# Performance work log

Measured on AMD Instinct MI355X. Metric: run time of the kernel, lower is better.

The kernel has to match this reference:

```python
import jax, jax.numpy as jnp
from jax import lax
import numpy as np

B, L1, L2 = 64, 1024, 1024


def setup_inputs() -> dict:
    key = jax.random.key(0)
    ks = jax.random.split(key, 6)
    s1 = 1.0 / np.sqrt(L1)
    s2 = 1.0 / np.sqrt(L2)
    return {
        "a": jax.random.normal(ks[0], (B, L1), dtype=jnp.float32),
        "b": jax.random.normal(ks[1], (B, L2), dtype=jnp.float32),
        # nn.Linear(L1, L1) and nn.Linear(L2, L2) params (PyTorch default uniform init range)
        "W1": jax.random.uniform(ks[2], (L1, L1), jnp.float32, -s1, s1),
        "b1": jax.random.uniform(ks[3], (L1,), jnp.float32, -s1, s1),
        "W2": jax.random.uniform(ks[4], (L2, L2), jnp.float32, -s2, s2),
        "b2": jax.random.uniform(ks[5], (L2,), jnp.float32, -s2, s2),
    }


def _dtw_cost(cost):
    """DTW accumulated-cost DP for one [N, M] pairwise-cost matrix.

    R[i,j] = cost[i,j] + min(R[i-1,j-1], R[i-1,j], R[i,j-1]).
    The within-row dependency x[j] = c[j] + min(m[j], x[j-1]) is a min-plus
    prefix: x[j] = S[j] + cummin(m - S_{j-1}) with S = cumsum(c), which lets
    each row be computed in parallel (wavefront-equivalent vectorization).
    Returns the scalar DTW distance R[N-1, M-1].
    """
    dt = cost.dtype
    row0 = jnp.cumsum(cost[0])  # R[0, :]

    def step(prev_row, c_row):
        # m[j] = min(R[i-1, j], R[i-1, j-1]);  j=0 has no (i-1, j-1) neighbor
        shifted = jnp.concatenate([jnp.full((1,), jnp.inf, dt), prev_row[:-1]])
        m = jnp.minimum(prev_row, shifted)
        S = jnp.cumsum(c_row)
        S_prev = jnp.concatenate([jnp.zeros((1,), dt), S[:-1]])
        row = S + lax.associative_scan(jnp.minimum, m - S_prev)
        return row, None

    last_row, _ = lax.scan(step, row0, cost[1:])
    return last_row[-1]


def reference(a, b, W1, b1, W2, b2):
    # seq1 / seq2 linear projections over the time axis
    a_p = a @ W1.T + b1  # [B, L1]
    b_p = b @ W2.T + b2  # [B, L2]
    # squared-euclidean pairwise cost (scipy.sqeuclidean on scalar elements)
    cost = (a_p[:, :, None] - b_p[:, None, :]) ** 2  # [B, L1, L2]
    return jax.vmap(_dtw_cost)(cost)  # [B] DTW distances
```

## Files before the change

### kernel.cpp

```cpp
#include <hip/hip_runtime.h>
#include <math.h>


#define L 1024
#define BATCH 64

__global__ __launch_bounds__(256) void proj_kernel(
    const float* __restrict__ a, const float* __restrict__ b,
    const float* __restrict__ W1, const float* __restrict__ b1,
    const float* __restrict__ W2, const float* __restrict__ b2,
    float* __restrict__ ap, float* __restrict__ bp, int KC) {
  int part = blockIdx.x >> 7;
  int sub = blockIdx.x & 127;
  const float* X;
  const float* W;
  const float* bias;
  float* out;
  int i0;
  if (sub < 64) {
    X = a; W = W1; bias = b1; out = ap + part * BATCH * L; i0 = sub * 16;
  } else {
    X = b; W = W2; bias = b2; out = bp + part * BATCH * L; i0 = (sub - 64) * 16;
  }

  __shared__ float a_s[64][36];
  __shared__ float w_s[16][36];

  int tid = threadIdx.x;
  int lane_b = tid & 63;
  int iq = tid >> 6;

  float acc[4] = {0.f, 0.f, 0.f, 0.f};

  int kbeg = part * KC;
  int kend = kbeg + KC;
  for (int k0 = kbeg; k0 < kend; k0 += 32) {
    {
      int row = tid >> 2;
      int kl = (tid & 3) * 8;
      const float4* src = reinterpret_cast<const float4*>(&X[row * L + k0 + kl]);
      float4 v0 = src[0];
      float4 v1 = src[1];
      *reinterpret_cast<float4*>(&a_s[row][kl]) = v0;
      *reinterpret_cast<float4*>(&a_s[row][kl + 4]) = v1;
    }
    {
      int row = tid >> 4;
      int kl = (tid & 15) * 2;
      float2 v = *reinterpret_cast<const float2*>(&W[(i0 + row) * L + k0 + kl]);
      w_s[row][kl] = v.x;
      w_s[row][kl + 1] = v.y;
    }
    __syncthreads();
    #pragma unroll
    for (int kl = 0; kl < 32; kl += 4) {
      float4 av = *reinterpret_cast<const float4*>(&a_s[lane_b][kl]);
      #pragma unroll
      for (int m = 0; m < 4; ++m) {
        float4 wv = *reinterpret_cast<const float4*>(&w_s[iq * 4 + m][kl]);
        acc[m] += av.x * wv.x + av.y * wv.y + av.z * wv.z + av.w * wv.w;
      }
    }
    __syncthreads();
  }

  #pragma unroll
  for (int m = 0; m < 4; ++m) {
    int i = i0 + iq * 4 + m;
    float bv = (part == 0) ? bias[i] : 0.f;
    out[lane_b * L + i] = acc[m] + bv;
  }
}


#define NW 4
#define CPL 4
#define KBAR 32
#define OFF 95
#define DMAX (OFF * (NW - 1) + 63)
#define NG 43
#define NSTEPS (NG * KBAR)
#define APPAD (DMAX + NSTEPS + 64)

__device__ __forceinline__ float dpp_shr1_z(float v) {
  int r = __builtin_amdgcn_update_dpp(0, __float_as_int(v), 0x138, 0xf, 0xf,
                                      true);
  return __int_as_float(r);
}

__device__ __forceinline__ float dpp_shl1_z(float v) {
  int r = __builtin_amdgcn_update_dpp(0, __float_as_int(v), 0x130, 0xf, 0xf,
                                      true);
  return __int_as_float(r);
}

__device__ __forceinline__ float min3f(float x, float y, float z) {
  float r;
  asm("v_min3_f32 %0, %1, %2, %3" : "=v"(r) : "v"(x), "v"(y), "v"(z));
  return r;
}

__global__ __launch_bounds__(256, 1) void dtw_kernel(
    const float* __restrict__ app, const float* __restrict__ bpp,
    float* __restrict__ out, int parts) {
  const int b = blockIdx.x;
  const int tid = threadIdx.x;
  const int w = tid >> 6;
  const int t = tid & 63;
  const int woff = w * OFF;
  const int D = woff + t;
  const float INF = INFINITY;

  __shared__ float ap_pad[APPAD];
  __shared__ float ring[NW - 1][64];

  for (int idx = tid; idx < APPAD; idx += 256) {
    int src = idx - DMAX;
    float v = 0.f;
    if ((unsigned)src < (unsigned)L) {
      v = app[b * L + src];
      for (int p = 1; p < parts; ++p) v += app[p * BATCH * L + b * L + src];
    }
    ap_pad[idx] = v;
  }

  float4 bv = *reinterpret_cast<const float4*>(&bpp[b * L + tid * CPL]);
  for (int p = 1; p < parts; ++p) {
    float4 u = *reinterpret_cast<const float4*>(
        &bpp[p * BATCH * L + b * L + tid * CPL]);
    bv.x += u.x; bv.y += u.y; bv.z += u.z; bv.w += u.w;
  }
  const float bpv0 = bv.x, bpv1 = bv.y, bpv2 = bv.z, bpv3 = bv.w;

  float p0 = INF, p1 = INF, p2 = INF, p3 = INF;
  float right = INF, prev_left = INF;
  float vprod = INF;
  float ringchunk = INF;
  float apv = 0.f;
  float apchunk = 0.f;
  const bool lane0 = (t == 0);
  const bool lane63 = (t == 63);
  const int ap_base = DMAX - woff + t;

  __syncthreads();

#define DTW_GROUP(s0v, PRED, FIRSTG)                                         \
  {                                                                          \
    const int s0 = (s0v);                                                    \
    apchunk = ap_pad[ap_base + s0];                                          \
    if (w == 0)                                                              \
      ringchunk = ((FIRSTG) && lane0) ? 0.f : INF;                           \
    else if (t < KBAR)                                                       \
      ringchunk = ring[w - 1][(s0 - woff + t) & 63];                         \
    _Pragma("unroll")                                                        \
    for (int k = 0; k < KBAR; ++k) {                                         \
      float shifted = dpp_shr1_z(right);                                     \
      float left = lane0 ? ringchunk : shifted;                              \
      ringchunk = dpp_shl1_z(ringchunk);                                     \
      float apsh = dpp_shr1_z(apv);                                          \
      apv = lane0 ? apchunk : apsh;                                          \
      apchunk = dpp_shl1_z(apchunk);                                         \
      int ii = s0 + k - D;                                                   \
      if (!(PRED) || ((unsigned)ii < (unsigned)L)) {                         \
        float dprev = prev_left;                                             \
        if ((FIRSTG) && k == 1 && w == 0 && t == 0) dprev = INF;             \
        prev_left = left;                                                    \
        float d0 = apv - bpv0, d1 = apv - bpv1;                              \
        float d2 = apv - bpv2, d3 = apv - bpv3;                              \
        float x = left, bb;                                                  \
        bb = min3f(p0, dprev, x); x = __builtin_fmaf(d0, d0, bb);            \
        dprev = p0; p0 = x;                                                  \
        bb = min3f(p1, dprev, x); x = __builtin_fmaf(d1, d1, bb);            \
        dprev = p1; p1 = x;                                                  \
        bb = min3f(p2, dprev, x); x = __builtin_fmaf(d2, d2, bb);            \
        dprev = p2; p2 = x;                                                  \
        bb = min3f(p3, dprev, x); x = __builtin_fmaf(d3, d3, bb);            \
        p3 = x;                                                              \
        right = x;                                                           \
      }                                                                      \
      vprod = dpp_shl1_z(vprod);                                             \
      vprod = lane63 ? right : vprod;                                        \
    }                                                                        \
    if (w < NW - 1 && t >= 64 - KBAR)                                        \
      ring[w][(s0 + t - woff - (63 + KBAR)) & 63] = vprod;                   \
    __syncthreads();                                                         \
  }

  for (int g = 0; g < 11; ++g) DTW_GROUP(g * KBAR, true, g == 0);
  for (int g = 11; g < 32; ++g) DTW_GROUP(g * KBAR, false, false);
  for (int g = 32; g < NG; ++g) DTW_GROUP(g * KBAR, true, false);
#undef DTW_GROUP

  if (tid == NW * 64 - 1) out[b] = right;
}

extern "C" void kernel_launch(void* const* d_in, const int* in_sizes, int n_in,
                              void* d_out, int out_size, void* d_ws, size_t ws_size,
                              hipStream_t stream) {
  const float* a  = (const float*)d_in[0];
  const float* b  = (const float*)d_in[1];
  const float* W1 = (const float*)d_in[2];
  const float* b1 = (const float*)d_in[3];
  const float* W2 = (const float*)d_in[4];
  const float* b2 = (const float*)d_in[5];
  float* out = (float*)d_out;

  size_t per_part = (size_t)2 * BATCH * L * sizeof(float);
  int parts = 1;
  if (ws_size >= 4 * per_part) parts = 4;
  else if (ws_size >= 2 * per_part) parts = 2;

  float* ap = (float*)d_ws;
  float* bp = ap + (size_t)parts * BATCH * L;

  proj_kernel<<<128 * parts, 256, 0, stream>>>(a, b, W1, b1, W2, b2,
                                               ap, bp, L / parts);
  dtw_kernel<<<BATCH, 256, 0, stream>>>(ap, bp, out, parts);
}
```

Before: 101.3 us.

## Use min-plus prefix form for per-lane DTW cells and preload ap values

Rewrites the four-cell serial min3+fma chain per lane as a min-plus prefix computation, cumsum of costs plus a cummin of shifted minima. This shortens the dependency chain through the incoming left value so only the last min+add depends on the neighbour lane. It also drops the per-step DPP shifting of the a-projection value and instead loads all KBAR values for a group from shared memory into registers up front. The cost is more instructions per step, more register pressure, and slightly different float rounding because the subtract-then-add reassociation is not exact.

```diff
diff --git a/kernel.cpp b/kernel.cpp
--- a/kernel.cpp
+++ b/kernel.cpp
@@ -94,12 +94,6 @@
   return __int_as_float(r);
 }
 
-__device__ __forceinline__ float min3f(float x, float y, float z) {
-  float r;
-  asm("v_min3_f32 %0, %1, %2, %3" : "=v"(r) : "v"(x), "v"(y), "v"(z));
-  return r;
-}
-
 __global__ __launch_bounds__(256, 1) void dtw_kernel(
     const float* __restrict__ app, const float* __restrict__ bpp,
     float* __restrict__ out, int parts) {
@@ -136,18 +130,18 @@
   float right = INF, prev_left = INF;
   float vprod = INF;
   float ringchunk = INF;
-  float apv = 0.f;
-  float apchunk = 0.f;
   const bool lane0 = (t == 0);
   const bool lane63 = (t == 63);
-  const int ap_base = DMAX - woff + t;
+  const float* apl = &ap_pad[DMAX - D];
 
   __syncthreads();
 
 #define DTW_GROUP(s0v, PRED, FIRSTG)                                         \
   {                                                                          \
     const int s0 = (s0v);                                                    \
-    apchunk = ap_pad[ap_base + s0];                                          \
+    float apf[KBAR];                                                         \
+    _Pragma("unroll")                                                        \
+    for (int k = 0; k < KBAR; ++k) apf[k] = apl[s0 + k];                     \
     if (w == 0)                                                              \
       ringchunk = ((FIRSTG) && lane0) ? 0.f : INF;                           \
     else if (t < KBAR)                                                       \
@@ -157,26 +151,31 @@
       float shifted = dpp_shr1_z(right);                                     \
       float left = lane0 ? ringchunk : shifted;                              \
       ringchunk = dpp_shl1_z(ringchunk);                                     \
-      float apsh = dpp_shr1_z(apv);                                          \
-      apv = lane0 ? apchunk : apsh;                                          \
-      apchunk = dpp_shl1_z(apchunk);                                         \
       int ii = s0 + k - D;                                                   \
       if (!(PRED) || ((unsigned)ii < (unsigned)L)) {                         \
         float dprev = prev_left;                                             \
         if ((FIRSTG) && k == 1 && w == 0 && t == 0) dprev = INF;             \
         prev_left = left;                                                    \
+        float apv = apf[k];                                                  \
         float d0 = apv - bpv0, d1 = apv - bpv1;                              \
         float d2 = apv - bpv2, d3 = apv - bpv3;                              \
-        float x = left, bb;                                                  \
-        bb = min3f(p0, dprev, x); x = __builtin_fmaf(d0, d0, bb);            \
-        dprev = p0; p0 = x;                                                  \
-        bb = min3f(p1, dprev, x); x = __builtin_fmaf(d1, d1, bb);            \
-        dprev = p1; p1 = x;                                                  \
-        bb = min3f(p2, dprev, x); x = __builtin_fmaf(d2, d2, bb);            \
-        dprev = p2; p2 = x;                                                  \
-        bb = min3f(p3, dprev, x); x = __builtin_fmaf(d3, d3, bb);            \
-        p3 = x;                                                              \
-        right = x;                                                           \
+        float c0 = d0 * d0, c1 = d1 * d1, c2 = d2 * d2, c3 = d3 * d3;        \
+        float S0 = c0, S1 = S0 + c1, S2 = S1 + c2, S3 = S2 + c3;             \
+        float m0 = fminf(p0, dprev);                                         \
+        float m1 = fminf(p1, p0);                                            \
+        float m2 = fminf(p2, p1);                                            \
+        float m3 = fminf(p3, p2);                                            \
+        float z0 = m0;                                                       \
+        float z1 = m1 - S0, z2 = m2 - S1, z3 = m3 - S2;                      \
+        float u01 = fminf(z0, z1);                                           \
+        float v23 = fminf(z2, z3);                                           \
+        float cm2 = fminf(u01, z2);                                          \
+        float cm3 = fminf(u01, v23);                                         \
+        p0 = S0 + fminf(z0, left);                                           \
+        p1 = S1 + fminf(u01, left);                                          \
+        p2 = S2 + fminf(cm2, left);                                          \
+        p3 = S3 + fminf(cm3, left);                                          \
+        right = p3;                                                          \
       }                                                                      \
       vprod = dpp_shl1_z(vprod);                                             \
       vprod = lane63 ? right : vprod;                                        \
```

Result: slower. 131.2 us (+29.5%).

## Interleave two batch DTW problems per block and load ap from LDS directly

Applied to the files above, without the earlier changes.

Each DTW block now processes two batch elements at once, interleaving their independent dependency chains so the latency of each serial min3/fma chain can be overlapped by the other. The per-step DPP shift of the a-projection value is replaced by per-lane LDS reads of a 32-entry chunk into registers. The change halves the grid to 32 blocks and roughly doubles register and LDS use per block, so GPU occupancy drops further.

```diff
diff --git a/kernel.cpp b/kernel.cpp
--- a/kernel.cpp
+++ b/kernel.cpp
@@ -103,7 +103,8 @@
 __global__ __launch_bounds__(256, 1) void dtw_kernel(
     const float* __restrict__ app, const float* __restrict__ bpp,
     float* __restrict__ out, int parts) {
-  const int b = blockIdx.x;
+  const int bA = blockIdx.x * 2;
+  const int bB = bA + 1;
   const int tid = threadIdx.x;
   const int w = tid >> 6;
   const int t = tid & 63;
@@ -111,78 +112,114 @@
   const int D = woff + t;
   const float INF = INFINITY;
 
-  __shared__ float ap_pad[APPAD];
-  __shared__ float ring[NW - 1][64];
+  __shared__ float ap_pad[2][APPAD];
+  __shared__ float ring[2][NW - 1][64];
 
   for (int idx = tid; idx < APPAD; idx += 256) {
     int src = idx - DMAX;
-    float v = 0.f;
+    float vA = 0.f, vB = 0.f;
     if ((unsigned)src < (unsigned)L) {
-      v = app[b * L + src];
-      for (int p = 1; p < parts; ++p) v += app[p * BATCH * L + b * L + src];
-    }
-    ap_pad[idx] = v;
-  }
-
-  float4 bv = *reinterpret_cast<const float4*>(&bpp[b * L + tid * CPL]);
+      vA = app[bA * L + src];
+      vB = app[bB * L + src];
+      for (int p = 1; p < parts; ++p) {
+        vA += app[p * BATCH * L + bA * L + src];
+        vB += app[p * BATCH * L + bB * L + src];
+      }
+    }
+    ap_pad[0][idx] = vA;
+    ap_pad[1][idx] = vB;
+  }
+
+  float4 bvA = *reinterpret_cast<const float4*>(&bpp[bA * L + tid * CPL]);
+  float4 bvB = *reinterpret_cast<const float4*>(&bpp[bB * L + tid * CPL]);
   for (int p = 1; p < parts; ++p) {
-    float4 u = *reinterpret_cast<const float4*>(
-        &bpp[p * BATCH * L + b * L + tid * CPL]);
-    bv.x += u.x; bv.y += u.y; bv.z += u.z; bv.w += u.w;
-  }
-  const float bpv0 = bv.x, bpv1 = bv.y, bpv2 = bv.z, bpv3 = bv.w;
-
-  float p0 = INF, p1 = INF, p2 = INF, p3 = INF;
-  float right = INF, prev_left = INF;
-  float vprod = INF;
-  float ringchunk = INF;
-  float apv = 0.f;
-  float apchunk = 0.f;
+    float4 uA = *reinterpret_cast<const float4*>(
+        &bpp[p * BATCH * L + bA * L + tid * CPL]);
+    float4 uB = *reinterpret_cast<const float4*>(
+        &bpp[p * BATCH * L + bB * L + tid * CPL]);
+    bvA.x += uA.x; bvA.y += uA.y; bvA.z += uA.z; bvA.w += uA.w;
+    bvB.x += uB.x; bvB.y += uB.y; bvB.z += uB.z; bvB.w += uB.w;
+  }
+  const float bpv0A = bvA.x, bpv1A = bvA.y, bpv2A = bvA.z, bpv3A = bvA.w;
+  const float bpv0B = bvB.x, bpv1B = bvB.y, bpv2B = bvB.z, bpv3B = bvB.w;
+
+  float p0A = INF, p1A = INF, p2A = INF, p3A = INF;
+  float p0B = INF, p1B = INF, p2B = INF, p3B = INF;
+  float rightA = INF, prev_leftA = INF, vprodA = INF, ringchunkA = INF;
+  float rightB = INF, prev_leftB = INF, vprodB = INF, ringchunkB = INF;
   const bool lane0 = (t == 0);
   const bool lane63 = (t == 63);
-  const int ap_base = DMAX - woff + t;
+  const float* aplA = &ap_pad[0][DMAX - D];
+  const float* aplB = &ap_pad[1][DMAX - D];
 
   __syncthreads();
 
 #define DTW_GROUP(s0v, PRED, FIRSTG)                                         \
   {                                                                          \
     const int s0 = (s0v);                                                    \
-    apchunk = ap_pad[ap_base + s0];                                          \
-    if (w == 0)                                                              \
-      ringchunk = ((FIRSTG) && lane0) ? 0.f : INF;                           \
-    else if (t < KBAR)                                                       \
-      ringchunk = ring[w - 1][(s0 - woff + t) & 63];                         \
+    float apfA[KBAR], apfB[KBAR];                                            \
     _Pragma("unroll")                                                        \
     for (int k = 0; k < KBAR; ++k) {                                         \
-      float shifted = dpp_shr1_z(right);                                     \
-      float left = lane0 ? ringchunk : shifted;                              \
-      ringchunk = dpp_shl1_z(ringchunk);                                     \
-      float apsh = dpp_shr1_z(apv);                                          \
-      apv = lane0 ? apchunk : apsh;                                          \
-      apchunk = dpp_shl1_z(apchunk);                                         \
+      apfA[k] = aplA[s0 + k];                                                \
+      apfB[k] = aplB[s0 + k];                                                \
+    }                                                                        \
+    if (w == 0) {                                                            \
+      ringchunkA = ((FIRSTG) && lane0) ? 0.f : INF;                          \
+      ringchunkB = ((FIRSTG) && lane0) ? 0.f : INF;                          \
+    } else if (t < KBAR) {                                                   \
+      ringchunkA = ring[0][w - 1][(s0 - woff + t) & 63];                     \
+      ringchunkB = ring[1][w - 1][(s0 - woff + t) & 63];                     \
+    }                                                                        \
+    _Pragma("unroll")                                                        \
+    for (int k = 0; k < KBAR; ++k) {                                         \
+      float shiftedA = dpp_shr1_z(rightA);                                   \
+      float shiftedB = dpp_shr1_z(rightB);                                   \
+      float leftA = lane0 ? ringchunkA : shiftedA;                           \
+      float leftB = lane0 ? ringchunkB : shiftedB;                           \
+      ringchunkA = dpp_shl1_z(ringchunkA);                                   \
+      ringchunkB = dpp_shl1_z(ringchunkB);                                   \
       int ii = s0 + k - D;                                                   \
       if (!(PRED) || ((unsigned)ii < (unsigned)L)) {                         \
-        float dprev = prev_left;                                             \
-        if ((FIRSTG) && k == 1 && w == 0 && t == 0) dprev = INF;             \
-        prev_left = left;                                                    \
-        float d0 = apv - bpv0, d1 = apv - bpv1;                              \
-        float d2 = apv - bpv2, d3 = apv - bpv3;                              \
-        float x = left, bb;                                                  \
-        bb = min3f(p0, dprev, x); x = __builtin_fmaf(d0, d0, bb);            \
-        dprev = p0; p0 = x;                                                  \
-        bb = min3f(p1, dprev, x); x = __builtin_fmaf(d1, d1, bb);            \
-        dprev = p1; p1 = x;                                                  \
-        bb = min3f(p2, dprev, x); x = __builtin_fmaf(d2, d2, bb);            \
-        dprev = p2; p2 = x;                                                  \
-        bb = min3f(p3, dprev, x); x = __builtin_fmaf(d3, d3, bb);            \
-        p3 = x;                                                              \
-        right = x;                                                           \
+        float dprevA = prev_leftA;                                           \
+        float dprevB = prev_leftB;                                           \
+        if ((FIRSTG) && k == 1 && w == 0 && t == 0) {                        \
+          dprevA = INF;                                                      \
+          dprevB = INF;                                                      \
+        }                                                                    \
+        prev_leftA = leftA;                                                  \
+        prev_leftB = leftB;                                                  \
+        float apvA = apfA[k], apvB = apfB[k];                                \
+        float d0A = apvA - bpv0A, d1A = apvA - bpv1A;                        \
+        float d2A = apvA - bpv2A, d3A = apvA - bpv3A;                        \
+        float d0B = apvB - bpv0B, d1B = apvB - bpv1B;                        \
+        float d2B = apvB - bpv2B, d3B = apvB - bpv3B;                        \
+        float xA = leftA, xB = leftB, bbA, bbB;                              \
+        bbA = min3f(p0A, dprevA, xA); xA = __builtin_fmaf(d0A, d0A, bbA);    \
+        bbB = min3f(p0B, dprevB, xB); xB = __builtin_fmaf(d0B, d0B, bbB);    \
+        dprevA = p0A; p0A = xA;                                              \
+        dprevB = p0B; p0B = xB;                                              \
+        bbA = min3f(p1A, dprevA, xA); xA = __builtin_fmaf(d1A, d1A, bbA);    \
+        bbB = min3f(p1B, dprevB, xB); xB = __builtin_fmaf(d1B, d1B, bbB);    \
+        dprevA = p1A; p1A = xA;                                              \
+        dprevB = p1B; p1B = xB;                                              \
+        bbA = min3f(p2A, dprevA, xA); xA = __builtin_fmaf(d2A, d2A, bbA);    \
+        bbB = min3f(p2B, dprevB, xB); xB = __builtin_fmaf(d2B, d2B, bbB);    \
+        dprevA = p2A; p2A = xA;                                              \
+        dprevB = p2B; p2B = xB;                                              \
+        bbA = min3f(p3A, dprevA, xA); xA = __builtin_fmaf(d3A, d3A, bbA);    \
+        bbB = min3f(p3B, dprevB, xB); xB = __builtin_fmaf(d3B, d3B, bbB);    \
+        p3A = xA; rightA = xA;                                               \
+        p3B = xB; rightB = xB;                                               \
       }                                                                      \
-      vprod = dpp_shl1_z(vprod);                                             \
-      vprod = lane63 ? right : vprod;                                        \
-    }                                                                        \
-    if (w < NW - 1 && t >= 64 - KBAR)                                        \
-      ring[w][(s0 + t - woff - (63 + KBAR)) & 63] = vprod;                   \
+      vprodA = dpp_shl1_z(vprodA);                                           \
+      vprodB = dpp_shl1_z(vprodB);                                           \
+      vprodA = lane63 ? rightA : vprodA;                                     \
+      vprodB = lane63 ? rightB : vprodB;                                     \
+    }                                                                        \
+    if (w < NW - 1 && t >= 64 - KBAR) {                                      \
+      ring[0][w][(s0 + t - woff - (63 + KBAR)) & 63] = vprodA;               \
+      ring[1][w][(s0 + t - woff - (63 + KBAR)) & 63] = vprodB;               \
+    }                                                                        \
     __syncthreads();                                                         \
   }
 
@@ -191,7 +228,10 @@
   for (int g = 32; g < NG; ++g) DTW_GROUP(g * KBAR, true, false);
 #undef DTW_GROUP
 
-  if (tid == NW * 64 - 1) out[b] = right;
+  if (tid == NW * 64 - 1) {
+    out[bA] = rightA;
+    out[bB] = rightB;
+  }
 }
 
 extern "C" void kernel_launch(void* const* d_in, const int* in_sizes, int n_in,
@@ -215,5 +255,5 @@
 
   proj_kernel<<<128 * parts, 256, 0, stream>>>(a, b, W1, b1, W2, b2,
                                                ap, bp, L / parts);
-  dtw_kernel<<<BATCH, 256, 0, stream>>>(ap, bp, out, parts);
-}
+  dtw_kernel<<<BATCH / 2, 256, 0, stream>>>(ap, bp, out, parts);
+}
```

Result: slower. 148.4 us (+46.4%).

## Pack two DTW batches per block and load ap values directly from LDS

Applied to the files above, without the earlier changes.

The DTW kernel now runs two batch elements per 512-thread block (32 blocks instead of 64), each half using its own LDS ap buffer and ring. The per-step DPP shifting of ap values is replaced by loading 32 ap values per group straight from shared memory into registers. This trims the DPP and select work in the serial inner loop, but the block-wide barriers now couple two independent problems. It also halves the number of CUs in use and raises register pressure from the 32-element array.

```diff
diff --git a/kernel.cpp b/kernel.cpp
--- a/kernel.cpp
+++ b/kernel.cpp
@@ -100,34 +100,44 @@
   return r;
 }
 
-__global__ __launch_bounds__(256, 1) void dtw_kernel(
+__global__ __launch_bounds__(512, 1) void dtw_kernel(
     const float* __restrict__ app, const float* __restrict__ bpp,
     float* __restrict__ out, int parts) {
-  const int b = blockIdx.x;
   const int tid = threadIdx.x;
-  const int w = tid >> 6;
+  const int q = tid >> 8;
+  const int wl = (tid >> 6) & 3;
   const int t = tid & 63;
-  const int woff = w * OFF;
+  const int bq = blockIdx.x * 2 + q;
+  const int woff = wl * OFF;
   const int D = woff + t;
   const float INF = INFINITY;
 
-  __shared__ float ap_pad[APPAD];
-  __shared__ float ring[NW - 1][64];
-
-  for (int idx = tid; idx < APPAD; idx += 256) {
-    int src = idx - DMAX;
-    float v = 0.f;
-    if ((unsigned)src < (unsigned)L) {
-      v = app[b * L + src];
-      for (int p = 1; p < parts; ++p) v += app[p * BATCH * L + b * L + src];
-    }
-    ap_pad[idx] = v;
-  }
-
-  float4 bv = *reinterpret_cast<const float4*>(&bpp[b * L + tid * CPL]);
+  __shared__ float ap_pad[2][APPAD];
+  __shared__ float ring[2][NW - 1][64];
+
+  {
+    const int bA = blockIdx.x * 2;
+    for (int idx = tid; idx < APPAD; idx += 512) {
+      int src = idx - DMAX;
+      float vA = 0.f, vB = 0.f;
+      if ((unsigned)src < (unsigned)L) {
+        vA = app[bA * L + src];
+        vB = app[(bA + 1) * L + src];
+        for (int p = 1; p < parts; ++p) {
+          vA += app[p * BATCH * L + bA * L + src];
+          vB += app[p * BATCH * L + (bA + 1) * L + src];
+        }
+      }
+      ap_pad[0][idx] = vA;
+      ap_pad[1][idx] = vB;
+    }
+  }
+
+  const int colb = (tid & 255) * CPL;
+  float4 bv = *reinterpret_cast<const float4*>(&bpp[bq * L + colb]);
   for (int p = 1; p < parts; ++p) {
     float4 u = *reinterpret_cast<const float4*>(
-        &bpp[p * BATCH * L + b * L + tid * CPL]);
+        &bpp[p * BATCH * L + bq * L + colb]);
     bv.x += u.x; bv.y += u.y; bv.z += u.z; bv.w += u.w;
   }
   const float bpv0 = bv.x, bpv1 = bv.y, bpv2 = bv.z, bpv3 = bv.w;
@@ -136,35 +146,33 @@
   float right = INF, prev_left = INF;
   float vprod = INF;
   float ringchunk = INF;
-  float apv = 0.f;
-  float apchunk = 0.f;
   const bool lane0 = (t == 0);
   const bool lane63 = (t == 63);
-  const int ap_base = DMAX - woff + t;
+  const float* apl = &ap_pad[q][DMAX - D];
 
   __syncthreads();
 
 #define DTW_GROUP(s0v, PRED, FIRSTG)                                         \
   {                                                                          \
     const int s0 = (s0v);                                                    \
-    apchunk = ap_pad[ap_base + s0];                                          \
-    if (w == 0)                                                              \
+    float apf[KBAR];                                                         \
+    _Pragma("unroll")                                                        \
+    for (int k = 0; k < KBAR; ++k) apf[k] = apl[s0 + k];                     \
+    if (wl == 0)                                                             \
       ringchunk = ((FIRSTG) && lane0) ? 0.f : INF;                           \
     else if (t < KBAR)                                                       \
-      ringchunk = ring[w - 1][(s0 - woff + t) & 63];                         \
+      ringchunk = ring[q][wl - 1][(s0 - woff + t) & 63];                     \
     _Pragma("unroll")                                                        \
     for (int k = 0; k < KBAR; ++k) {                                         \
       float shifted = dpp_shr1_z(right);                                     \
       float left = lane0 ? ringchunk : shifted;                              \
       ringchunk = dpp_shl1_z(ringchunk);                                     \
-      float apsh = dpp_shr1_z(apv);                                          \
-      apv = lane0 ? apchunk : apsh;                                          \
-      apchunk = dpp_shl1_z(apchunk);                                         \
       int ii = s0 + k - D;                                                   \
       if (!(PRED) || ((unsigned)ii < (unsigned)L)) {                         \
         float dprev = prev_left;                                             \
-        if ((FIRSTG) && k == 1 && w == 0 && t == 0) dprev = INF;             \
+        if ((FIRSTG) && k == 1 && wl == 0 && t == 0) dprev = INF;            \
         prev_left = left;                                                    \
+        float apv = apf[k];                                                  \
         float d0 = apv - bpv0, d1 = apv - bpv1;                              \
         float d2 = apv - bpv2, d3 = apv - bpv3;                              \
         float x = left, bb;                                                  \
@@ -181,8 +189,8 @@
       vprod = dpp_shl1_z(vprod);                                             \
       vprod = lane63 ? right : vprod;                                        \
     }                                                                        \
-    if (w < NW - 1 && t >= 64 - KBAR)                                        \
-      ring[w][(s0 + t - woff - (63 + KBAR)) & 63] = vprod;                   \
+    if (wl < NW - 1 && t >= 64 - KBAR)                                       \
+      ring[q][wl][(s0 + t - woff - (63 + KBAR)) & 63] = vprod;               \
     __syncthreads();                                                         \
   }
 
@@ -191,7 +199,7 @@
   for (int g = 32; g < NG; ++g) DTW_GROUP(g * KBAR, true, false);
 #undef DTW_GROUP
 
-  if (tid == NW * 64 - 1) out[b] = right;
+  if ((tid & 255) == 255) out[bq] = right;
 }
 
 extern "C" void kernel_launch(void* const* d_in, const int* in_sizes, int n_in,
@@ -215,5 +223,5 @@
 
   proj_kernel<<<128 * parts, 256, 0, stream>>>(a, b, W1, b1, W2, b2,
                                                ap, bp, L / parts);
-  dtw_kernel<<<BATCH, 256, 0, stream>>>(ap, bp, out, parts);
-}
+  dtw_kernel<<<BATCH / 2, 512, 0, stream>>>(ap, bp, out, parts);
+}
```

Result: slower. 122.0 us (+20.4%).
